# Kernel tuning notes

Hardware: AMD Instinct MI355X
Metric: run time of the kernel (lower is better)

Reference implementation:

```python
import jax, jax.numpy as jnp
import numpy as np
from math import sqrt

N = 8192
INPUT_SIZE = 256
D_MODEL = 256


def setup_inputs() -> dict:
    key = jax.random.key(0)
    k1, k2, k3, k4 = jax.random.split(key, 4)
    x = jax.random.normal(k1, (N, INPUT_SIZE), dtype=jnp.float32)
    adj = jax.random.randint(k2, (N, N), 0, 2, dtype=jnp.int32)
    # torch nn.Linear(input_size, d_model): weight [d_model, input_size], bias [d_model]
    bound = 1.0 / sqrt(INPUT_SIZE)
    Vw = jax.random.uniform(k3, (D_MODEL, INPUT_SIZE), dtype=jnp.float32, minval=-bound, maxval=bound)
    Vb = jax.random.uniform(k4, (D_MODEL,), dtype=jnp.float32, minval=-bound, maxval=bound)
    return {"x": x, "adj": adj, "Vw": Vw, "Vb": Vb}


def reference(x, adj, Vw, Vb):
    # value = V(x)
    value = x @ Vw.T + Vb                                  # [N, d_model]
    # scores = x x^T / sqrt(d_model), masked where adj == 0
    scores = (x @ x.T) * (1.0 / sqrt(D_MODEL))             # [N, N]
    scores = jnp.where(adj == 0, jnp.float32(-1e9), scores)
    p_attn = jax.nn.softmax(scores, axis=-1)               # [N, N]
    Vs = p_attn @ value                                    # [N, d_model]
    return (Vs, p_attn)
```

## Files before the change

kernel.cpp:

```cpp
#include <hip/hip_runtime.h>
#include <hip/hip_bf16.h>


#define NN 8192
#define DD 256

typedef __attribute__((ext_vector_type(8))) short bf16x8;
typedef __attribute__((ext_vector_type(8))) unsigned short u16x8;
typedef __attribute__((ext_vector_type(4))) float f32x4;
typedef __attribute__((ext_vector_type(4))) int i32x4;

__device__ __forceinline__ unsigned short f2bf(float f) {
  unsigned u = __builtin_bit_cast(unsigned, f);
  u += 0x7fffu + ((u >> 16) & 1u);
  return (unsigned short)(u >> 16);
}
__device__ __forceinline__ float bf2f(unsigned short h) {
  unsigned u = ((unsigned)h) << 16;
  return __builtin_bit_cast(float, u);
}
__device__ __forceinline__ unsigned pack2(float a, float b) {
  return (unsigned)f2bf(a) | ((unsigned)f2bf(b) << 16);
}

__global__ void k_prep_x(const float* __restrict__ x, unsigned short* __restrict__ xb) {
  int t = blockIdx.x * 256 + threadIdx.x;
  const float4* s = reinterpret_cast<const float4*>(x) + (size_t)t * 2;
  float4 f0 = s[0], f1 = s[1];
  uint4 o;
  o.x = pack2(f0.x, f0.y); o.y = pack2(f0.z, f0.w);
  o.z = pack2(f1.x, f1.y); o.w = pack2(f1.z, f1.w);
  reinterpret_cast<uint4*>(xb)[t] = o;
}

__global__ void k_prep_adj(const int* __restrict__ adj, unsigned char* __restrict__ adjp) {
  size_t t = (size_t)blockIdx.x * 256 + threadIdx.x;
  const i32x4* s = reinterpret_cast<const i32x4*>(adj) + t * 2;
  i32x4 v0 = __builtin_nontemporal_load(s);
  i32x4 v1 = __builtin_nontemporal_load(s + 1);
  unsigned b = 0;
  b |= (v0[0] != 0) ? 1u : 0u;  b |= (v0[1] != 0) ? 2u : 0u;
  b |= (v0[2] != 0) ? 4u : 0u;  b |= (v0[3] != 0) ? 8u : 0u;
  b |= (v1[0] != 0) ? 16u : 0u; b |= (v1[1] != 0) ? 32u : 0u;
  b |= (v1[2] != 0) ? 64u : 0u; b |= (v1[3] != 0) ? 128u : 0u;
  adjp[t] = (unsigned char)b;
}

__global__ __launch_bounds__(256) void k_value(
    const float* __restrict__ Vw, const float* __restrict__ Vb,
    const unsigned short* __restrict__ xb, unsigned short* __restrict__ vT) {
  __shared__ unsigned short lB[64 * 256];
  int mb = blockIdx.x >> 2, nb = blockIdx.x & 3;
  int tid = threadIdx.x, lane = tid & 63, w = tid >> 6;
  int mw = w >> 1, nw = w & 1;
  {
    int n_l = tid >> 2, q = tid & 3;
#pragma unroll
    for (int o = 0; o < 8; ++o) {
      int k0 = q * 64 + o * 8;
      const float4* src = reinterpret_cast<const float4*>(Vw + (nb * 64 + n_l) * DD + k0);
      float4 g0 = src[0], g1 = src[1];
      uint4 pk;
      pk.x = pack2(g0.x, g0.y); pk.y = pack2(g0.z, g0.w);
      pk.z = pack2(g1.x, g1.y); pk.w = pack2(g1.z, g1.w);
      *reinterpret_cast<uint4*>(reinterpret_cast<char*>(lB) + n_l * 512 + ((k0 * 2) ^ ((n_l & 7) << 4))) = pk;
    }
  }
  bf16x8 aR[2][8];
#pragma unroll
  for (int mf = 0; mf < 2; ++mf) {
    int rg = mb * 64 + mw * 32 + mf * 16 + (lane & 15);
    const char* base = reinterpret_cast<const char*>(xb + (size_t)rg * DD);
#pragma unroll
    for (int ks = 0; ks < 8; ++ks)
      aR[mf][ks] = *reinterpret_cast<const bf16x8*>(base + ks * 64 + ((lane >> 4) * 16));
  }
  __syncthreads();
  f32x4 acc[2][2] = {};
#pragma unroll
  for (int ks = 0; ks < 8; ++ks) {
    int kb = ks * 64 + ((lane >> 4) * 16);
#pragma unroll
    for (int nf = 0; nf < 2; ++nf) {
      int n = nw * 32 + nf * 16 + (lane & 15);
      bf16x8 b = *reinterpret_cast<const bf16x8*>(reinterpret_cast<const char*>(lB) + n * 512 + (kb ^ ((n & 7) << 4)));
#pragma unroll
      for (int mf = 0; mf < 2; ++mf)
        acc[mf][nf] = __builtin_amdgcn_mfma_f32_16x16x32_bf16(aR[mf][ks], b, acc[mf][nf], 0, 0, 0);
    }
  }
#pragma unroll
  for (int nf = 0; nf < 2; ++nf) {
    int n_g = nb * 64 + nw * 32 + nf * 16 + (lane & 15);
    float vb = Vb[n_g];
#pragma unroll
    for (int mf = 0; mf < 2; ++mf) {
      int m_g = mb * 64 + mw * 32 + mf * 16 + ((lane >> 4) << 2);
      ushort4 h;
      h.x = f2bf(acc[mf][nf][0] + vb);
      h.y = f2bf(acc[mf][nf][1] + vb);
      h.z = f2bf(acc[mf][nf][2] + vb);
      h.w = f2bf(acc[mf][nf][3] + vb);
      *reinterpret_cast<ushort4*>(vT + (size_t)n_g * NN + m_g) = h;
    }
  }
}

__global__ __launch_bounds__(256) void k_pass1(
    const unsigned short* __restrict__ xb, const unsigned long long* __restrict__ adjp,
    unsigned short* __restrict__ ews, float* __restrict__ lpart) {
  __shared__ char smem[65536];
  int rb = blockIdx.x >> 6, cb = blockIdx.x & 63;
  int tid = threadIdx.x, lane = tid & 63, w = tid >> 6;
  int mw = w >> 1, wc = w & 1;
  int ln = lane & 15, kq = lane >> 4;
#pragma unroll
  for (int c = 0; c < 16; ++c) {
    int id = c * 256 + tid;
    int col = id >> 5, oct = id & 31;
    uint4 v = *reinterpret_cast<const uint4*>(xb + (size_t)(cb * 128 + col) * DD + oct * 8);
    *reinterpret_cast<uint4*>(smem + col * 512 + ((oct * 16) ^ ((col & 7) << 4))) = v;
  }
  bf16x8 aR[2][8];
#pragma unroll
  for (int mf = 0; mf < 2; ++mf) {
    int rg = rb * 64 + mw * 32 + mf * 16 + ln;
    const char* base = reinterpret_cast<const char*>(xb + (size_t)rg * DD);
#pragma unroll
    for (int ks = 0; ks < 8; ++ks)
      aR[mf][ks] = *reinterpret_cast<const bf16x8*>(base + ks * 64 + kq * 16);
  }
  __syncthreads();
  int r0 = rb * 64 + mw * 32 + (kq << 2);
  unsigned long long mrow[2][4];
#pragma unroll
  for (int mf = 0; mf < 2; ++mf)
#pragma unroll
    for (int i = 0; i < 4; ++i)
      mrow[mf][i] = adjp[(size_t)(r0 + mf * 16 + i) * 128 + cb * 2 + wc];
  f32x4 acc[2][4] = {};
#pragma unroll
  for (int ks = 0; ks < 8; ++ks) {
    int kb = ks * 64 + kq * 16;
#pragma unroll
    for (int nf = 0; nf < 4; ++nf) {
      int cc = wc * 64 + nf * 16 + ln;
      bf16x8 b = *reinterpret_cast<const bf16x8*>(smem + cc * 512 + (kb ^ ((cc & 7) << 4)));
#pragma unroll
      for (int mf = 0; mf < 2; ++mf)
        acc[mf][nf] = __builtin_amdgcn_mfma_f32_16x16x32_bf16(aR[mf][ks], b, acc[mf][nf], 0, 0, 0);
    }
  }
  int c0 = cb * 128 + wc * 64 + ln;
#pragma unroll
  for (int mf = 0; mf < 2; ++mf)
#pragma unroll
    for (int nf = 0; nf < 4; ++nf)
#pragma unroll
      for (int i = 0; i < 4; ++i) {
        bool on = (mrow[mf][i] >> (nf * 16 + ln)) & 1;
        float e = on ? __expf(acc[mf][nf][i] * 0.0625f) : 0.f;
        unsigned short h = f2bf(e);
        ews[(size_t)(r0 + mf * 16 + i) * NN + (c0 + nf * 16)] = h;
        acc[mf][nf][i] = bf2f(h);
      }
  __syncthreads();
  float* ls = reinterpret_cast<float*>(smem);
#pragma unroll
  for (int mf = 0; mf < 2; ++mf)
#pragma unroll
    for (int i = 0; i < 4; ++i) {
      float r = acc[mf][0][i] + acc[mf][1][i] + acc[mf][2][i] + acc[mf][3][i];
      r += __shfl_xor(r, 1); r += __shfl_xor(r, 2);
      r += __shfl_xor(r, 4); r += __shfl_xor(r, 8);
      if (ln == 0)
        ls[wc * 64 + mw * 32 + mf * 16 + (kq << 2) + i] = r;
    }
  __syncthreads();
  if (tid < 64)
    lpart[(size_t)cb * NN + rb * 64 + tid] = ls[tid] + ls[64 + tid];
}

__global__ void k_reduce_l(const float* __restrict__ lpart, float* __restrict__ rl) {
  int i = blockIdx.x * 256 + threadIdx.x;
  float s = 0.f;
  for (int c = 0; c < 64; ++c) s += lpart[(size_t)c * NN + i];
  rl[i] = s > 0.f ? 1.f / s : 0.f;
}

__global__ __launch_bounds__(512) void k_vs(
    const unsigned short* __restrict__ ews, const unsigned short* __restrict__ vT,
    const float* __restrict__ rl, unsigned short* __restrict__ vspb) {
  __shared__ char lV[2][65536];
  int rt = blockIdx.x >> 2, ck = blockIdx.x & 3;
  int tid = threadIdx.x, lane = tid & 63, w = tid >> 6;
  int ln = lane & 15, kq = lane >> 4;
  int row = rt * 128 + w * 16 + ln;
  const unsigned short* ap = ews + (size_t)row * NN + ck * 2048 + kq * 8;

#define LOADB(G, KC)                                                                     \
  _Pragma("unroll") for (int q = 0; q < 8; ++q) {                                        \
    int id_ = q * 512 + tid, n_ = id_ >> 4, o_ = id_ & 15;                               \
    (G)[q] = *reinterpret_cast<const uint4*>(vT + (size_t)n_ * NN + ck * 2048 + (KC) * 128 + o_ * 8); \
  }
#define DSWRITE(G, BB)                                                                   \
  _Pragma("unroll") for (int q = 0; q < 8; ++q) {                                        \
    int id_ = q * 512 + tid, n_ = id_ >> 4, o_ = id_ & 15;                               \
    *reinterpret_cast<uint4*>(&lV[BB][n_ * 256 + ((o_ * 16) ^ ((n_ & 7) << 4))]) = (G)[q]; \
  }
#define LOADA(A, KC)                                                                     \
  _Pragma("unroll") for (int s_ = 0; s_ < 4; ++s_)                                       \
    (A)[s_] = __builtin_nontemporal_load(reinterpret_cast<const bf16x8*>(ap + (KC) * 128 + s_ * 32));

  uint4 gB[8];
  bf16x8 aC[4], aN[4];
  LOADB(gB, 0);
  LOADA(aC, 0);
  DSWRITE(gB, 0);
  __syncthreads();

  f32x4 acc[16] = {};
  for (int kc = 0; kc < 16; ++kc) {
    bool has = kc < 15;
    if (has) {
      LOADB(gB, kc + 1);
      LOADA(aN, kc + 1);
    }
    const char* bufc = lV[kc & 1];
#pragma unroll
    for (int ks = 0; ks < 4; ++ks) {
#pragma unroll
      for (int nf = 0; nf < 16; ++nf) {
        int n = nf * 16 + ln;
        bf16x8 b = *reinterpret_cast<const bf16x8*>(bufc + n * 256 + ((ks * 64 + kq * 16) ^ ((n & 7) << 4)));
        acc[nf] = __builtin_amdgcn_mfma_f32_16x16x32_bf16(aC[ks], b, acc[nf], 0, 0, 0);
      }
    }
    if (has) DSWRITE(gB, (kc + 1) & 1);
    __syncthreads();
#pragma unroll
    for (int s = 0; s < 4; ++s) aC[s] = aN[s];
  }

  int rowo = rt * 128 + w * 16 + kq * 4;
#pragma unroll
  for (int i = 0; i < 4; ++i) {
    float rli = rl[rowo + i];
#pragma unroll
    for (int nf = 0; nf < 16; ++nf) {
      int n = nf * 16 + ln;
      vspb[((size_t)ck * NN + rowo + i) * DD + n] = f2bf(acc[nf][i] * rli);
    }
  }
#undef LOADB
#undef DSWRITE
#undef LOADA
}

__global__ void k_norm(const unsigned short* __restrict__ ews, const float* __restrict__ rl,
                       float* __restrict__ pout) {
  size_t t = (size_t)blockIdx.x * 256 + threadIdx.x;
  float r = rl[t >> 10];
  u16x8 v = __builtin_nontemporal_load(reinterpret_cast<const u16x8*>(ews + t * 8));
  f32x4 o0, o1;
  o0[0] = bf2f(v[0]) * r; o0[1] = bf2f(v[1]) * r; o0[2] = bf2f(v[2]) * r; o0[3] = bf2f(v[3]) * r;
  o1[0] = bf2f(v[4]) * r; o1[1] = bf2f(v[5]) * r; o1[2] = bf2f(v[6]) * r; o1[3] = bf2f(v[7]) * r;
  f32x4* pd = reinterpret_cast<f32x4*>(pout + t * 8);
  __builtin_nontemporal_store(o0, pd);
  __builtin_nontemporal_store(o1, pd + 1);
}

__global__ void k_reduce_vs(const unsigned short* __restrict__ vspb, float* __restrict__ vout) {
  int t = blockIdx.x * 256 + threadIdx.x;
  float s[8] = {};
#pragma unroll
  for (int c = 0; c < 4; ++c) {
    u16x8 v = *reinterpret_cast<const u16x8*>(vspb + (size_t)c * NN * DD + (size_t)t * 8);
#pragma unroll
    for (int j = 0; j < 8; ++j) s[j] += bf2f(v[j]);
  }
  float4 o0, o1;
  o0.x = s[0]; o0.y = s[1]; o0.z = s[2]; o0.w = s[3];
  o1.x = s[4]; o1.y = s[5]; o1.z = s[6]; o1.w = s[7];
  float4* d = reinterpret_cast<float4*>(vout + (size_t)t * 8);
  d[0] = o0; d[1] = o1;
}

extern "C" void kernel_launch(void* const* d_in, const int* in_sizes, int n_in,
                              void* d_out, int out_size, void* d_ws, size_t ws_size,
                              hipStream_t stream) {
  const float* x   = (const float*)d_in[0];
  const int*   adj = (const int*)d_in[1];
  const float* Vw  = (const float*)d_in[2];
  const float* Vb  = (const float*)d_in[3];
  float* out   = (float*)d_out;
  float* vs_out = out;
  float* p_out  = out + (size_t)NN * DD;
  char* ws = (char*)d_ws;
  unsigned short* xb   = (unsigned short*)(ws);
  unsigned short* vT   = (unsigned short*)(ws + ((size_t)4  << 20));
  float* rl            = (float*)(ws + ((size_t)8  << 20));
  float* lpart         = (float*)(ws + ((size_t)9  << 20));
  unsigned short* vspb = (unsigned short*)(ws + ((size_t)11 << 20));
  unsigned short* ews  = (unsigned short*)(ws + ((size_t)27 << 20));
  unsigned char* adjp  = (unsigned char*)(ws + ((size_t)156 << 20));

  k_prep_x<<<dim3(1024), dim3(256), 0, stream>>>(x, xb);
  k_prep_adj<<<dim3(32768), dim3(256), 0, stream>>>(adj, adjp);
  k_value<<<dim3(512), dim3(256), 0, stream>>>(Vw, Vb, xb, vT);
  k_pass1<<<dim3(8192), dim3(256), 0, stream>>>(xb, (const unsigned long long*)adjp, ews, lpart);
  k_reduce_l<<<dim3(32), dim3(256), 0, stream>>>(lpart, rl);
  k_vs<<<dim3(256), dim3(512), 0, stream>>>(ews, vT, rl, vspb);
  k_norm<<<dim3(32768), dim3(256), 0, stream>>>(ews, rl, p_out);
  k_reduce_vs<<<dim3(1024), dim3(256), 0, stream>>>(vspb, vs_out);
}
```

Before: 364.6 us.

## Restructure score pass into persistent double-buffered column loop per block

The score/exp pass now gives each 512-thread block 128 rows and a 1024-column strip. It loops over 16 column chunks of 64, double-buffering the B tile in LDS with register prefetch, and keeps A fragments resident. Row sums accumulate in registers across chunks, so the partial-sum array shrinks from 64 to 8 slices and the reduction kernel reads fewer partials. This cuts redundant A loads and per-block setup, and overlaps global loads with MFMA work. In exchange there are far fewer blocks (512), so latency hiding depends on the in-block pipeline, and there is a barrier per chunk.

```diff
diff --git a/kernel.cpp b/kernel.cpp
--- a/kernel.cpp
+++ b/kernel.cpp
@@ -106,85 +106,89 @@
   }
 }
 
-__global__ __launch_bounds__(256) void k_pass1(
+__global__ __launch_bounds__(512, 4) void k_pass1(
     const unsigned short* __restrict__ xb, const unsigned long long* __restrict__ adjp,
     unsigned short* __restrict__ ews, float* __restrict__ lpart) {
-  __shared__ char smem[65536];
-  int rb = blockIdx.x >> 6, cb = blockIdx.x & 63;
+  __shared__ char lB[2][32768];
+  int cs = blockIdx.x >> 6, rb = blockIdx.x & 63;
   int tid = threadIdx.x, lane = tid & 63, w = tid >> 6;
-  int mw = w >> 1, wc = w & 1;
   int ln = lane & 15, kq = lane >> 4;
-#pragma unroll
-  for (int c = 0; c < 16; ++c) {
-    int id = c * 256 + tid;
-    int col = id >> 5, oct = id & 31;
-    uint4 v = *reinterpret_cast<const uint4*>(xb + (size_t)(cb * 128 + col) * DD + oct * 8);
-    *reinterpret_cast<uint4*>(smem + col * 512 + ((oct * 16) ^ ((col & 7) << 4))) = v;
-  }
-  bf16x8 aR[2][8];
-#pragma unroll
-  for (int mf = 0; mf < 2; ++mf) {
-    int rg = rb * 64 + mw * 32 + mf * 16 + ln;
-    const char* base = reinterpret_cast<const char*>(xb + (size_t)rg * DD);
+  int colb = cs * 1024;
+  int r0 = rb * 128 + w * 16 + (kq << 2);
+
+  bf16x8 aR[8];
+  {
+    const char* abase = reinterpret_cast<const char*>(xb + (size_t)(rb * 128 + w * 16 + ln) * DD);
 #pragma unroll
     for (int ks = 0; ks < 8; ++ks)
-      aR[mf][ks] = *reinterpret_cast<const bf16x8*>(base + ks * 64 + kq * 16);
-  }
+      aR[ks] = *reinterpret_cast<const bf16x8*>(abase + ks * 64 + kq * 16);
+  }
+
+#define LOADB(G, KC)                                                                   \
+  _Pragma("unroll") for (int q = 0; q < 4; ++q) {                                      \
+    int id_ = q * 512 + tid, col_ = id_ >> 5, oct_ = id_ & 31;                         \
+    (G)[q] = *reinterpret_cast<const uint4*>(xb + (size_t)(colb + (KC) * 64 + col_) * DD + oct_ * 8); \
+  }
+#define DSWRITE(G, BB)                                                                 \
+  _Pragma("unroll") for (int q = 0; q < 4; ++q) {                                      \
+    int id_ = q * 512 + tid, col_ = id_ >> 5, oct_ = id_ & 31;                         \
+    *reinterpret_cast<uint4*>(&lB[BB][col_ * 512 + ((oct_ * 16) ^ ((col_ & 7) << 4))]) = (G)[q]; \
+  }
+
+  uint4 gB[4];
+  LOADB(gB, 0);
+  DSWRITE(gB, 0);
   __syncthreads();
-  int r0 = rb * 64 + mw * 32 + (kq << 2);
-  unsigned long long mrow[2][4];
-#pragma unroll
-  for (int mf = 0; mf < 2; ++mf)
+
+  float rsum[4] = {};
+  for (int kc = 0; kc < 16; ++kc) {
+    bool has = kc < 15;
+    if (has) LOADB(gB, kc + 1);
+    unsigned long long m[4];
 #pragma unroll
     for (int i = 0; i < 4; ++i)
-      mrow[mf][i] = adjp[(size_t)(r0 + mf * 16 + i) * 128 + cb * 2 + wc];
-  f32x4 acc[2][4] = {};
-#pragma unroll
-  for (int ks = 0; ks < 8; ++ks) {
-    int kb = ks * 64 + kq * 16;
-#pragma unroll
-    for (int nf = 0; nf < 4; ++nf) {
-      int cc = wc * 64 + nf * 16 + ln;
-      bf16x8 b = *reinterpret_cast<const bf16x8*>(smem + cc * 512 + (kb ^ ((cc & 7) << 4)));
-#pragma unroll
-      for (int mf = 0; mf < 2; ++mf)
-        acc[mf][nf] = __builtin_amdgcn_mfma_f32_16x16x32_bf16(aR[mf][ks], b, acc[mf][nf], 0, 0, 0);
-    }
-  }
-  int c0 = cb * 128 + wc * 64 + ln;
-#pragma unroll
-  for (int mf = 0; mf < 2; ++mf)
+      m[i] = adjp[(size_t)(r0 + i) * 128 + cs * 16 + kc];
+    const char* bufc = lB[kc & 1];
+    f32x4 acc[4] = {};
+#pragma unroll
+    for (int ks = 0; ks < 8; ++ks) {
+      int kb = ks * 64 + kq * 16;
+#pragma unroll
+      for (int nf = 0; nf < 4; ++nf) {
+        int cc = nf * 16 + ln;
+        bf16x8 b = *reinterpret_cast<const bf16x8*>(bufc + cc * 512 + (kb ^ ((cc & 7) << 4)));
+        acc[nf] = __builtin_amdgcn_mfma_f32_16x16x32_bf16(aR[ks], b, acc[nf], 0, 0, 0);
+      }
+    }
+    int c0 = colb + kc * 64 + ln;
 #pragma unroll
     for (int nf = 0; nf < 4; ++nf)
 #pragma unroll
       for (int i = 0; i < 4; ++i) {
-        bool on = (mrow[mf][i] >> (nf * 16 + ln)) & 1;
-        float e = on ? __expf(acc[mf][nf][i] * 0.0625f) : 0.f;
+        bool on = (m[i] >> (nf * 16 + ln)) & 1;
+        float e = on ? __expf(acc[nf][i] * 0.0625f) : 0.f;
         unsigned short h = f2bf(e);
-        ews[(size_t)(r0 + mf * 16 + i) * NN + (c0 + nf * 16)] = h;
-        acc[mf][nf][i] = bf2f(h);
+        ews[(size_t)(r0 + i) * NN + c0 + nf * 16] = h;
+        rsum[i] += bf2f(h);
       }
-  __syncthreads();
-  float* ls = reinterpret_cast<float*>(smem);
-#pragma unroll
-  for (int mf = 0; mf < 2; ++mf)
-#pragma unroll
-    for (int i = 0; i < 4; ++i) {
-      float r = acc[mf][0][i] + acc[mf][1][i] + acc[mf][2][i] + acc[mf][3][i];
-      r += __shfl_xor(r, 1); r += __shfl_xor(r, 2);
-      r += __shfl_xor(r, 4); r += __shfl_xor(r, 8);
-      if (ln == 0)
-        ls[wc * 64 + mw * 32 + mf * 16 + (kq << 2) + i] = r;
-    }
-  __syncthreads();
-  if (tid < 64)
-    lpart[(size_t)cb * NN + rb * 64 + tid] = ls[tid] + ls[64 + tid];
+    if (has) DSWRITE(gB, (kc + 1) & 1);
+    __syncthreads();
+  }
+#pragma unroll
+  for (int i = 0; i < 4; ++i) {
+    float r = rsum[i];
+    r += __shfl_xor(r, 1); r += __shfl_xor(r, 2);
+    r += __shfl_xor(r, 4); r += __shfl_xor(r, 8);
+    if (ln == 0) lpart[(size_t)cs * NN + r0 + i] = r;
+  }
+#undef LOADB
+#undef DSWRITE
 }
 
 __global__ void k_reduce_l(const float* __restrict__ lpart, float* __restrict__ rl) {
   int i = blockIdx.x * 256 + threadIdx.x;
   float s = 0.f;
-  for (int c = 0; c < 64; ++c) s += lpart[(size_t)c * NN + i];
+  for (int c = 0; c < 8; ++c) s += lpart[(size_t)c * NN + i];
   rl[i] = s > 0.f ? 1.f / s : 0.f;
 }
 
@@ -308,7 +312,7 @@
   k_prep_x<<<dim3(1024), dim3(256), 0, stream>>>(x, xb);
   k_prep_adj<<<dim3(32768), dim3(256), 0, stream>>>(adj, adjp);
   k_value<<<dim3(512), dim3(256), 0, stream>>>(Vw, Vb, xb, vT);
-  k_pass1<<<dim3(8192), dim3(256), 0, stream>>>(xb, (const unsigned long long*)adjp, ews, lpart);
+  k_pass1<<<dim3(512), dim3(512), 0, stream>>>(xb, (const unsigned long long*)adjp, ews, lpart);
   k_reduce_l<<<dim3(32), dim3(256), 0, stream>>>(lpart, rl);
   k_vs<<<dim3(256), dim3(512), 0, stream>>>(ews, vT, rl, vspb);
   k_norm<<<dim3(32768), dim3(256), 0, stream>>>(ews, rl, p_out);
```

Result: faster. 320.9 us (-12.0%).
